# Kernel optimization log

Hardware: AMD Instinct MI355X
Metric: run time of the kernel (lower is better)

Reference implementation:

```python
import jax, jax.numpy as jnp
import numpy as np

B, S, D = 8, 2048, 1024

def setup_inputs() -> dict:
    key = jax.random.key(0)
    ks = jax.random.split(key, 7)
    s = 1.0 / np.sqrt(D)
    return {
        "x": jax.random.normal(ks[0], (B, S, D), dtype=jnp.float32),
        "Wq": jax.random.normal(ks[1], (D, D), dtype=jnp.float32) * s,
        "bq": jnp.zeros((D,), dtype=jnp.float32),
        "Wk": jax.random.normal(ks[2], (D, D), dtype=jnp.float32) * s,
        "bk": jnp.zeros((D,), dtype=jnp.float32),
        "Wv": jax.random.normal(ks[3], (D, D), dtype=jnp.float32) * s,
        "bv": jnp.zeros((D,), dtype=jnp.float32),
    }

def reference(x, Wq, bq, Wk, bk, Wv, bv):
    # QKV projections: [B,S,D]
    q = x @ Wq + bq
    k = x @ Wk + bk
    v = x @ Wv + bv
    # scores scaled by sqrt(full input_dim) — single head, per source
    scores = jnp.einsum("bsd,btd->bst", q, k) / jnp.sqrt(jnp.float32(D))
    attn = jax.nn.softmax(scores, axis=2)
    return jnp.einsum("bst,btd->bsd", attn, v)
```

## Files before the change

kernel.cpp:

```cpp
#include <hip/hip_runtime.h>

typedef _Float16 half8 __attribute__((ext_vector_type(8)));
typedef float floatx4 __attribute__((ext_vector_type(4)));

#define AS1 __attribute__((address_space(1)))
#define AS3 __attribute__((address_space(3)))

__global__ __launch_bounds__(256) void wtrans_kernel(
    const float* __restrict__ W0, const float* __restrict__ W1,
    const float* __restrict__ W2, _Float16* __restrict__ Wt)
{
    __shared__ _Float16 t[64 * 72];
    const float* W = (blockIdx.z == 0) ? W0 : (blockIdx.z == 1) ? W1 : W2;
    _Float16* O = Wt + (long)blockIdx.z * 1048576;
    const int tid = threadIdx.x;
    const int kb = blockIdx.y * 64, nb = blockIdx.x * 64;
#pragma unroll
    for (int i = 0; i < 4; i++) {
        int r = (tid >> 4) + i * 16;
        int c = (tid & 15) * 4;
        floatx4 w = *(const floatx4*)&W[(long)(kb + r) * 1024 + nb + c];
#pragma unroll
        for (int j = 0; j < 4; j++) t[(c + j) * 72 + r] = (_Float16)w[j];
    }
    __syncthreads();
    const int c = tid >> 2, rch = (tid & 3) * 16;
    half8 v0 = *(const half8*)&t[c * 72 + rch];
    half8 v1 = *(const half8*)&t[c * 72 + rch + 8];
    _Float16* o = &O[(long)(nb + c) * 1024 + kb + rch];
    *(half8*)o = v0;
    *(half8*)(o + 8) = v1;
}

__global__ __launch_bounds__(256) void f32_to_f16_kernel(
    const float* __restrict__ in, _Float16* __restrict__ out, int n)
{
    for (long i = ((long)blockIdx.x * 256 + threadIdx.x) * 8; i < n;
         i += (long)gridDim.x * 256 * 8) {
        floatx4 a = *(const floatx4*)&in[i];
        floatx4 b = *(const floatx4*)&in[i + 4];
        half8 h;
#pragma unroll
        for (int e = 0; e < 4; e++) { h[e] = (_Float16)a[e]; h[e + 4] = (_Float16)b[e]; }
        *(half8*)&out[i] = h;
    }
}

template <int MODE>
__global__ __launch_bounds__(256) void gemm128_kernel(
    const _Float16* __restrict__ A, const _Float16* __restrict__ Bt,
    void* __restrict__ Cv, const float* __restrict__ bias,
    const float* __restrict__ bias2,
    int nx, int ny,
    int K, int lda, int ldb, int ldc,
    long aBatch, long bBatch, long cBatch, float scale)
{
    constexpr int SMEM_ELEMS = (MODE == 1) ? 17408 : 16384;
    __shared__ _Float16 smem[SMEM_ELEMS];
    _Float16* Ash = smem;
    _Float16* Bsh = smem + 8192;

    const int tid = threadIdx.x;
    const int wave = tid >> 6, lane = tid & 63;
    const int quad = lane >> 4, lr = lane & 15;
    const int wm = wave & 1, wn = wave >> 1;

    const int P = gridDim.x >> 3;
    const int g = (blockIdx.x & 7) * P + (blockIdx.x >> 3);
    const int pplane = nx * ny;
    const int z = g / pplane;
    const int rr = g - z * pplane;
    const int by = rr / nx;
    const int bx = rr - by * nx;
    const int m0 = by * 128, n0 = bx * 128;

    const _Float16* Ab = A + (long)z * aBatch;
    const _Float16* Bb = Bt + (long)z * bBatch;

    const int srow = tid >> 2;
    const int scol = (tid & 3) * 8;
    const long ag0 = (long)(m0 + srow) * lda + scol;
    const long bg0 = (long)(n0 + srow) * ldb + scol;
    const int sdst = tid * 8;

    floatx4 acc[4][4] = {};

    for (int k0 = 0; k0 < K; k0 += 64) {
#pragma unroll
        for (int s = 0; s < 2; s++) {
            const int kk = k0 + s * 32;
            const int so = s * 4096;
            __builtin_amdgcn_global_load_lds(
                (AS1 void*)(Ab + ag0 + kk), (AS3 void*)(Ash + so + sdst), 16, 0, 0);
            __builtin_amdgcn_global_load_lds(
                (AS1 void*)(Ab + ag0 + (long)64 * lda + kk), (AS3 void*)(Ash + so + sdst + 2048), 16, 0, 0);
            __builtin_amdgcn_global_load_lds(
                (AS1 void*)(Bb + bg0 + kk), (AS3 void*)(Bsh + so + sdst), 16, 0, 0);
            __builtin_amdgcn_global_load_lds(
                (AS1 void*)(Bb + bg0 + (long)64 * ldb + kk), (AS3 void*)(Bsh + so + sdst + 2048), 16, 0, 0);
        }
        __syncthreads();

#pragma unroll
        for (int s = 0; s < 2; s++) {
            const int so = s * 4096;
            half8 aF[4], bF[4];
#pragma unroll
            for (int i = 0; i < 4; i++) {
                aF[i] = *(const half8*)&Ash[so + (wm * 64 + i * 16 + lr) * 32 + quad * 8];
                bF[i] = *(const half8*)&Bsh[so + (wn * 64 + i * 16 + lr) * 32 + quad * 8];
            }
#pragma unroll
            for (int mi = 0; mi < 4; mi++)
#pragma unroll
                for (int ni = 0; ni < 4; ni++)
                    acc[mi][ni] = __builtin_amdgcn_mfma_f32_16x16x32_f16(
                        aF[mi], bF[ni], acc[mi][ni], 0, 0, 0);
        }
        __syncthreads();
    }

    if constexpr (MODE == 0) {
        _Float16* C = (_Float16*)Cv + (long)z * cBatch;
        const float* bz = (z == 0 || !bias2) ? bias : bias2;
#pragma unroll
        for (int ni = 0; ni < 4; ni++) {
            const int n = n0 + wn * 64 + ni * 16 + lr;
            const float bv_ = bz ? bz[n] : 0.0f;
#pragma unroll
            for (int mi = 0; mi < 4; mi++) {
                const int mb = m0 + wm * 64 + mi * 16 + quad * 4;
#pragma unroll
                for (int r = 0; r < 4; r++)
                    C[(long)(mb + r) * ldc + n] = (_Float16)((acc[mi][ni][r] + bv_) * scale);
            }
        }
    } else if constexpr (MODE == 1) {
        _Float16* ctile = smem;
#pragma unroll
        for (int ni = 0; ni < 4; ni++) {
            const int nl = wn * 64 + ni * 16 + lr;
            const float bv_ = bias ? bias[n0 + nl] : 0.0f;
#pragma unroll
            for (int mi = 0; mi < 4; mi++) {
                const int ml = wm * 64 + mi * 16 + quad * 4;
#pragma unroll
                for (int r = 0; r < 4; r++)
                    ctile[nl * 136 + ml + r] = (_Float16)((acc[mi][ni][r] + bv_) * scale);
            }
        }
        __syncthreads();
        _Float16* C = (_Float16*)Cv + (long)(m0 >> 11) * cBatch;
        const int t0 = m0 & 2047;
#pragma unroll
        for (int p = 0; p < 8; p++) {
            const int row = p * 16 + (tid >> 4);
            const int seg = (tid & 15) * 8;
            half8 v = *(const half8*)&ctile[row * 136 + seg];
            *(half8*)&C[(long)(n0 + row) * ldc + t0 + seg] = v;
        }
    } else {
        float* C = (float*)Cv + (long)z * cBatch;
#pragma unroll
        for (int ni = 0; ni < 4; ni++) {
            const int n = n0 + wn * 64 + ni * 16 + lr;
#pragma unroll
            for (int mi = 0; mi < 4; mi++) {
                const int mb = m0 + wm * 64 + mi * 16 + quad * 4;
#pragma unroll
                for (int r = 0; r < 4; r++)
                    C[(long)(mb + r) * ldc + n] = acc[mi][ni][r] * scale;
            }
        }
    }
}

__global__ __launch_bounds__(256) void softmax_kernel(_Float16* __restrict__ buf)
{
    const int lane = threadIdx.x & 63;
    const long row = (long)blockIdx.x * 4 + (threadIdx.x >> 6);
    _Float16* p = buf + row * 2048;

    float f[32];
#pragma unroll
    for (int j = 0; j < 4; j++) {
        half8 v = *(const half8*)&p[lane * 8 + j * 512];
#pragma unroll
        for (int e = 0; e < 8; e++) f[j * 8 + e] = (float)v[e];
    }
    float m = -1e30f;
#pragma unroll
    for (int i = 0; i < 32; i++) m = fmaxf(m, f[i]);
#pragma unroll
    for (int off = 32; off; off >>= 1) m = fmaxf(m, __shfl_xor(m, off, 64));
    float s = 0.0f;
#pragma unroll
    for (int i = 0; i < 32; i++) { f[i] = __expf(f[i] - m); s += f[i]; }
#pragma unroll
    for (int off = 32; off; off >>= 1) s += __shfl_xor(s, off, 64);
    const float inv = 1.0f / s;
#pragma unroll
    for (int j = 0; j < 4; j++) {
        half8 v;
#pragma unroll
        for (int e = 0; e < 8; e++) v[e] = (_Float16)(f[j * 8 + e] * inv);
        *(half8*)&p[lane * 8 + j * 512] = v;
    }
}

extern "C" void kernel_launch(void* const* d_in, const int* in_sizes, int n_in,
                              void* d_out, int out_size, void* d_ws, size_t ws_size,
                              hipStream_t stream)
{
    const float* x  = (const float*)d_in[0];
    const float* Wq = (const float*)d_in[1];
    const float* bq = (const float*)d_in[2];
    const float* Wk = (const float*)d_in[3];
    const float* bk = (const float*)d_in[4];
    const float* Wv = (const float*)d_in[5];
    const float* bv = (const float*)d_in[6];

    if (ws_size < 174063616u) return;

    char* ws = (char*)d_ws;
    _Float16* Q  = (_Float16*)(ws + 0);
    _Float16* Vt = (_Float16*)(ws + 67108864);
    _Float16* Sc = (_Float16*)(ws + 100663296);
    _Float16* Wt = (_Float16*)(ws + 167772160);
    _Float16* xb = Sc;
    _Float16* Kb = Q + 16777216;
    float* out = (float*)d_out;

    wtrans_kernel<<<dim3(16, 16, 3), 256, 0, stream>>>(Wq, Wk, Wv, Wt);
    f32_to_f16_kernel<<<2048, 256, 0, stream>>>(x, xb, 16777216);

    gemm128_kernel<0><<<2048, 256, 0, stream>>>(
        xb, Wt, Q, bq, bk, 8, 128, 1024, 1024, 1024, 1024,
        0, 1048576, 16777216, 1.0f);
    gemm128_kernel<1><<<1024, 256, 0, stream>>>(
        xb, Wt + 2097152, Vt, bv, nullptr, 8, 128, 1024, 1024, 1024, 2048,
        0, 0, 2097152, 1.0f);

    gemm128_kernel<0><<<2048, 256, 0, stream>>>(
        Q, Kb, Sc, nullptr, nullptr, 16, 16, 1024, 1024, 1024, 2048,
        2097152, 2097152, 4194304, 0.03125f);

    softmax_kernel<<<4096, 256, 0, stream>>>(Sc);

    gemm128_kernel<2><<<1024, 256, 0, stream>>>(
        Sc, Vt, out, nullptr, nullptr, 8, 16, 2048, 2048, 2048, 1024,
        4194304, 2097152, 2097152, 1.0f);
}
```

Baseline: 463.0 us.

## Add 256x256-tile 8-wave GEMM with phased LDS pipelining for QK, scores, PV

Adds a new GEMM kernel using 256x256 output tiles with 512 threads. It stages A and B tiles into double-buffered LDS through direct global-to-LDS loads and interleaves four MFMA quarter-phases with the next tile's loads, using barriers and s_setprio. Three of the four GEMM launches (QK projection, score GEMM, PV GEMM) switch to it, which gives more data reuse per tile and better overlap of memory with compute. In exchange it needs 128KB of LDS, uses more registers and launches fewer blocks, which may leave some CUs underused.

Result: faster. 446.6 us (-3.5%).

```diff
diff --git a/kernel.cpp b/kernel.cpp
--- a/kernel.cpp
+++ b/kernel.cpp
@@ -175,6 +175,174 @@
     }
 }
 
+#define STAGE_A(d, h, kt) do { \
+    __builtin_amdgcn_global_load_lds((AS1 void*)(Ap + (long)((h) * 64) * lda + (long)(kt) * 64), \
+        (AS3 void*)(Ash + (d) * 16384 + (h) * 8192 + sdst), 16, 0, 0); \
+    __builtin_amdgcn_global_load_lds((AS1 void*)(Ap + (long)((h) * 64 + 128) * lda + (long)(kt) * 64), \
+        (AS3 void*)(Ash + (d) * 16384 + (h) * 8192 + 4096 + sdst), 16, 0, 0); \
+} while (0)
+
+#define STAGE_B(d, h, kt) do { \
+    __builtin_amdgcn_global_load_lds((AS1 void*)(Bp0 + (long)((h) * 32) * ldb + (long)(kt) * 64), \
+        (AS3 void*)(Bsh + (d) * 16384 + (h) * 8192 + sdst), 16, 0, 0); \
+    __builtin_amdgcn_global_load_lds((AS1 void*)(Bp1 + (long)((h) * 32) * ldb + (long)(kt) * 64), \
+        (AS3 void*)(Bsh + (d) * 16384 + (h) * 8192 + 4096 + sdst), 16, 0, 0); \
+} while (0)
+
+#define LDA_FRAGS(d, mh) do { \
+    _Pragma("unroll") for (int mi_ = 0; mi_ < 4; mi_++) { \
+        const _Float16* p_ = &Ash[(d) * 16384 + (mh) * 8192 + (arow + mi_ * 16) * 64]; \
+        aF[mi_][0] = *(const half8*)&p_[kq0]; \
+        aF[mi_][1] = *(const half8*)&p_[kq1]; \
+    } \
+} while (0)
+
+#define LDB_FRAGS(d, nh) do { \
+    _Pragma("unroll") for (int ni_ = 0; ni_ < 2; ni_++) { \
+        const _Float16* p_ = &Bsh[(d) * 16384 + (nh) * 8192 + (brow + ni_ * 16) * 64]; \
+        bF[nh][ni_][0] = *(const half8*)&p_[kq0]; \
+        bF[nh][ni_][1] = *(const half8*)&p_[kq1]; \
+    } \
+} while (0)
+
+#define MFMA16(mh, nh) do { \
+    __builtin_amdgcn_s_setprio(1); \
+    _Pragma("unroll") for (int mi_ = 0; mi_ < 4; mi_++) \
+    _Pragma("unroll") for (int ni_ = 0; ni_ < 2; ni_++) { \
+        acc[(mh) * 4 + mi_][(nh) * 2 + ni_] = __builtin_amdgcn_mfma_f32_16x16x32_f16( \
+            aF[mi_][0], bF[nh][ni_][0], acc[(mh) * 4 + mi_][(nh) * 2 + ni_], 0, 0, 0); \
+        acc[(mh) * 4 + mi_][(nh) * 2 + ni_] = __builtin_amdgcn_mfma_f32_16x16x32_f16( \
+            aF[mi_][1], bF[nh][ni_][1], acc[(mh) * 4 + mi_][(nh) * 2 + ni_], 0, 0, 0); \
+    } \
+    __builtin_amdgcn_s_setprio(0); \
+} while (0)
+
+#define PHASE_SYNC() do { \
+    __builtin_amdgcn_s_barrier(); \
+    __builtin_amdgcn_sched_barrier(0); \
+} while (0)
+
+template <int MODE>
+__global__ __launch_bounds__(512, 2) void gemm256_kernel(
+    const _Float16* __restrict__ A, const _Float16* __restrict__ Bt,
+    void* __restrict__ Cv, const float* __restrict__ bias,
+    const float* __restrict__ bias2,
+    int nx, int ny, int K, int lda, int ldb, int ldc,
+    long aBatch, long bBatch, long cBatch, float scale)
+{
+    __shared__ _Float16 smem[65536];
+    _Float16* Ash = smem;
+    _Float16* Bsh = smem + 32768;
+
+    const int tid = threadIdx.x;
+    const int wave = tid >> 6, lane = tid & 63;
+    const int quad = lane >> 4, lr = lane & 15;
+    const int wm = wave >> 2, wn = wave & 3;
+
+    const int P = gridDim.x >> 3;
+    const int g = (blockIdx.x & 7) * P + (blockIdx.x >> 3);
+    const int pplane = nx * ny;
+    const int z = g / pplane;
+    const int rr = g - z * pplane;
+    const int by = rr / nx;
+    const int bx = rr - by * nx;
+    const int m0 = by * 256, n0 = bx * 256;
+
+    const _Float16* Ab = A + (long)z * aBatch;
+    const _Float16* Bb = Bt + (long)z * bBatch;
+
+    const int sr0 = tid >> 3;
+    const int sc0 = (tid & 7) ^ (sr0 & 7);
+    const _Float16* Ap = Ab + (long)(m0 + sr0) * lda + sc0 * 8;
+    const int bc0 = (sr0 & 31) + ((sr0 >> 5) << 6);
+    const int bc1 = (sr0 & 31) + (((sr0 >> 5) + 2) << 6);
+    const _Float16* Bp0 = Bb + (long)(n0 + bc0) * ldb + sc0 * 8;
+    const _Float16* Bp1 = Bb + (long)(n0 + bc1) * ldb + sc0 * 8;
+    const int sdst = tid * 8;
+
+    const int kq0 = (quad * 8) ^ ((lr & 7) << 3);
+    const int kq1 = (32 + quad * 8) ^ ((lr & 7) << 3);
+    const int arow = wm * 64 + lr;
+    const int brow = wn * 32 + lr;
+
+    half8 aF[4][2];
+    half8 bF[2][2][2];
+    floatx4 acc[8][4] = {};
+    const int NT = K >> 6;
+
+    STAGE_A(0, 0, 0); STAGE_A(0, 1, 0); STAGE_B(0, 0, 0); STAGE_B(0, 1, 0);
+    if (NT > 1) { STAGE_A(1, 0, 1); STAGE_B(1, 0, 1); }
+    asm volatile("s_waitcnt vmcnt(4)" ::: "memory");
+    __builtin_amdgcn_s_barrier();
+    __builtin_amdgcn_sched_barrier(0);
+
+    for (int t = 0; t < NT; t++) {
+        const int d = t & 1, dn = d ^ 1;
+        LDA_FRAGS(d, 0); LDB_FRAGS(d, 0);
+        if (t + 1 < NT) STAGE_A(dn, 1, t + 1);
+        PHASE_SYNC();
+        MFMA16(0, 0);
+        PHASE_SYNC();
+        LDB_FRAGS(d, 1);
+        if (t + 1 < NT) STAGE_B(dn, 1, t + 1);
+        PHASE_SYNC();
+        MFMA16(0, 1);
+        PHASE_SYNC();
+        LDA_FRAGS(d, 1);
+        if (t + 2 < NT) STAGE_A(d, 0, t + 2);
+        PHASE_SYNC();
+        MFMA16(1, 0);
+        PHASE_SYNC();
+        if (t + 2 < NT) STAGE_B(d, 0, t + 2);
+        PHASE_SYNC();
+        MFMA16(1, 1);
+        PHASE_SYNC();
+        if (t + 1 < NT) {
+            if (t + 2 < NT) asm volatile("s_waitcnt vmcnt(4)" ::: "memory");
+            else            asm volatile("s_waitcnt vmcnt(0)" ::: "memory");
+            __builtin_amdgcn_s_barrier();
+            __builtin_amdgcn_sched_barrier(0);
+        }
+    }
+
+    if constexpr (MODE == 0) {
+        _Float16* C = (_Float16*)Cv + (long)z * cBatch;
+        const float* bz = (z == 0 || !bias2) ? bias : bias2;
+#pragma unroll
+        for (int ni = 0; ni < 4; ni++) {
+            const int n = n0 + wn * 64 + ni * 16 + lr;
+            const float bv_ = bz ? bz[n] : 0.0f;
+#pragma unroll
+            for (int mi = 0; mi < 8; mi++) {
+                const int mb = m0 + wm * 128 + mi * 16 + quad * 4;
+#pragma unroll
+                for (int r = 0; r < 4; r++)
+                    C[(long)(mb + r) * ldc + n] = (_Float16)((acc[mi][ni][r] + bv_) * scale);
+            }
+        }
+    } else {
+        float* C = (float*)Cv + (long)z * cBatch;
+#pragma unroll
+        for (int ni = 0; ni < 4; ni++) {
+            const int n = n0 + wn * 64 + ni * 16 + lr;
+#pragma unroll
+            for (int mi = 0; mi < 8; mi++) {
+                const int mb = m0 + wm * 128 + mi * 16 + quad * 4;
+#pragma unroll
+                for (int r = 0; r < 4; r++)
+                    C[(long)(mb + r) * ldc + n] = acc[mi][ni][r] * scale;
+            }
+        }
+    }
+}
+
+#undef STAGE_A
+#undef STAGE_B
+#undef LDA_FRAGS
+#undef LDB_FRAGS
+#undef MFMA16
+#undef PHASE_SYNC
+
 __global__ __launch_bounds__(256) void softmax_kernel(_Float16* __restrict__ buf)
 {
     const int lane = threadIdx.x & 63;
@@ -234,20 +402,20 @@
     wtrans_kernel<<<dim3(16, 16, 3), 256, 0, stream>>>(Wq, Wk, Wv, Wt);
     f32_to_f16_kernel<<<2048, 256, 0, stream>>>(x, xb, 16777216);
 
-    gemm128_kernel<0><<<2048, 256, 0, stream>>>(
-        xb, Wt, Q, bq, bk, 8, 128, 1024, 1024, 1024, 1024,
+    gemm256_kernel<0><<<512, 512, 0, stream>>>(
+        xb, Wt, Q, bq, bk, 4, 64, 1024, 1024, 1024, 1024,
         0, 1048576, 16777216, 1.0f);
     gemm128_kernel<1><<<1024, 256, 0, stream>>>(
         xb, Wt + 2097152, Vt, bv, nullptr, 8, 128, 1024, 1024, 1024, 2048,
         0, 0, 2097152, 1.0f);
 
-    gemm128_kernel<0><<<2048, 256, 0, stream>>>(
-        Q, Kb, Sc, nullptr, nullptr, 16, 16, 1024, 1024, 1024, 2048,
+    gemm256_kernel<0><<<512, 512, 0, stream>>>(
+        Q, Kb, Sc, nullptr, nullptr, 8, 8, 1024, 1024, 1024, 2048,
         2097152, 2097152, 4194304, 0.03125f);
 
     softmax_kernel<<<4096, 256, 0, stream>>>(Sc);
 
-    gemm128_kernel<2><<<1024, 256, 0, stream>>>(
-        Sc, Vt, out, nullptr, nullptr, 8, 16, 2048, 2048, 2048, 1024,
+    gemm256_kernel<2><<<256, 512, 0, stream>>>(
+        Sc, Vt, out, nullptr, nullptr, 4, 8, 2048, 2048, 2048, 1024,
         4194304, 2097152, 2097152, 1.0f);
 }
```
